# Optimization experiments

Hardware: AMD Instinct MI355X
Metric: run time of the kernel (lower is better)

## Reference

```python
import jax, jax.numpy as jnp
import numpy as np

N_NODES = 50000
N_EDGES = 800000
NUM_GRAPHS = 256
IN = 128
HID = 256
NUM_CLASSES = 10
EPS = 1e-5


def _glorot(key, shape):
    fan_in, fan_out = shape[0], shape[1]
    lim = (6.0 / (fan_in + fan_out)) ** 0.5
    return jax.random.uniform(key, shape, jnp.float32, -lim, lim)


def setup_inputs() -> dict:
    key = jax.random.key(0)
    ks = jax.random.split(key, 32)
    x = jax.random.normal(ks[0], (N_NODES, IN), jnp.float32)
    edge_index = jax.random.randint(ks[1], (2, N_EDGES), 0, N_NODES, jnp.int64)
    batch = jnp.sort(jax.random.randint(ks[2], (N_NODES,), 0, NUM_GRAPHS, jnp.int64))
    h = IN // 2  # 64
    p = {
        "x": x, "edge_index": edge_index, "batch": batch,
        # SAGEConv: out = lin_l(mean_aggr(x_j)) + lin_r(x_i); lin_l has bias, lin_r none
        "W1l": _glorot(ks[3], (IN, h)), "b1l": jnp.zeros((h,), jnp.float32), "W1r": _glorot(ks[4], (IN, h)),
        "W2l": _glorot(ks[5], (h, h)), "b2l": jnp.zeros((h,), jnp.float32), "W2r": _glorot(ks[6], (h, h)),
        "W3l": _glorot(ks[7], (h, h)), "b3l": jnp.zeros((h,), jnp.float32), "W3r": _glorot(ks[8], (h, h)),
        "lin1_w": _glorot(ks[9], (h, HID)), "lin1_b": jnp.zeros((HID,), jnp.float32),
        "g1": jnp.ones((HID,), jnp.float32), "be1": jnp.zeros((HID,), jnp.float32),
        "lin2_w": _glorot(ks[10], (HID, HID // 2)), "lin2_b": jnp.zeros((HID // 2,), jnp.float32),
        "g2": jnp.ones((HID // 2,), jnp.float32), "be2": jnp.zeros((HID // 2,), jnp.float32),
        "lin3_w": _glorot(ks[11], (HID // 2, HID // 4)), "lin3_b": jnp.zeros((HID // 4,), jnp.float32),
        "g3": jnp.ones((HID // 4,), jnp.float32), "be3": jnp.zeros((HID // 4,), jnp.float32),
        "lin4_w": _glorot(ks[12], (HID // 4, NUM_CLASSES)), "lin4_b": jnp.zeros((NUM_CLASSES,), jnp.float32),
    }
    return p


def sage_conv(x, src, dst, Wl, bl, Wr):
    # mean aggregation of source-node messages at destination nodes
    msg = x[src]  # [E, d] gather
    agg = jax.ops.segment_sum(msg, dst, num_segments=N_NODES)
    cnt = jax.ops.segment_sum(jnp.ones((src.shape[0],), x.dtype), dst, num_segments=N_NODES)
    agg = agg / jnp.maximum(cnt, 1.0)[:, None]
    return agg @ Wl + bl + x @ Wr


def batch_norm(x, gamma, beta):
    # training-mode BN (batch statistics, biased variance) as in torch default
    mean = jnp.mean(x, axis=0)
    var = jnp.mean((x - mean) ** 2, axis=0)
    return (x - mean) / jnp.sqrt(var + EPS) * gamma + beta


def reference(x, edge_index, batch,
              W1l, b1l, W1r, W2l, b2l, W2r, W3l, b3l, W3r,
              lin1_w, lin1_b, g1, be1, lin2_w, lin2_b, g2, be2,
              lin3_w, lin3_b, g3, be3, lin4_w, lin4_b):
    src, dst = edge_index[0], edge_index[1]
    h = sage_conv(x, src, dst, W1l, b1l, W1r)
    h = sage_conv(h, src, dst, W2l, b2l, W2r)
    h = sage_conv(h, src, dst, W3l, b3l, W3r)
    # global_mean_pool over graphs
    s = jax.ops.segment_sum(h, batch, num_segments=NUM_GRAPHS)
    n = jax.ops.segment_sum(jnp.ones((h.shape[0],), h.dtype), batch, num_segments=NUM_GRAPHS)
    c = s / jnp.maximum(n, 1.0)[:, None]
    # dropout is identity (self.training = False)
    c = jnp.tanh(batch_norm(c @ lin1_w + lin1_b, g1, be1))
    c = jnp.tanh(batch_norm(c @ lin2_w + lin2_b, g2, be2))
    c = jnp.tanh(batch_norm(c @ lin3_w + lin3_b, g3, be3))
    return c @ lin4_w + lin4_b
```

## Files before the change

kernel.cpp:

```cpp
#include <hip/hip_runtime.h>
#include <hip/hip_bf16.h>

#define N_NODES   50000
#define N_EDGES   800000
#define NUM_GRAPHS 256
#define IN_DIM    128
#define HD        64
#define EPS       1e-5f
#define SCAN_NB   196
#define NB_HEAD   64

typedef __hip_bfloat16 bf16;

__global__ void k_diag(float* __restrict__ out, int n, float v) {
    int t = blockIdx.x * 256 + threadIdx.x;
    if (t < n) out[t] = v;
}

__global__ void k_count(const int* __restrict__ dst, const int* __restrict__ batch,
                        int* __restrict__ cnti, int* __restrict__ pos,
                        int* __restrict__ gb) {
    int e = blockIdx.x * 256 + threadIdx.x;
    if (e < N_EDGES) pos[e] = atomicAdd(&cnti[dst[e]], 1);
    if (e < N_NODES) {
        int bg = batch[e];
        int bnext = (e + 1 < N_NODES) ? batch[e + 1] : NUM_GRAPHS;
        if (e == 0) {
            for (int g = 0; g <= bg; ++g) gb[g] = 0;
        }
        for (int g = bg + 1; g <= bnext; ++g) gb[g] = e + 1;
    }
}

__global__ void k_scan1(const int* __restrict__ cnti, int* __restrict__ off,
                        int* __restrict__ bsum) {
    __shared__ int wsum[4];
    int idx = blockIdx.x * 256 + threadIdx.x;
    int lane = threadIdx.x & 63, wid = threadIdx.x >> 6;
    int v = (idx < N_NODES) ? cnti[idx] : 0;
    int s = v;
    #pragma unroll
    for (int o = 1; o < 64; o <<= 1) {
        int u = __shfl_up(s, o);
        if (lane >= o) s += u;
    }
    if (lane == 63) wsum[wid] = s;
    __syncthreads();
    int wbase = 0;
    #pragma unroll
    for (int w = 0; w < 4; w++) wbase += (w < wid) ? wsum[w] : 0;
    if (idx < N_NODES) off[idx] = wbase + s - v;
    if (threadIdx.x == 255) bsum[blockIdx.x] = wbase + s;
}

__global__ void k_scan3(int* __restrict__ off, const int* __restrict__ bsum) {
    __shared__ int wsum[4];
    __shared__ int spre;
    int lane = threadIdx.x & 63, wid = threadIdx.x >> 6;
    int v = (threadIdx.x < blockIdx.x) ? bsum[threadIdx.x] : 0;
    #pragma unroll
    for (int o = 32; o > 0; o >>= 1) v += __shfl_down(v, o);
    if (lane == 0) wsum[wid] = v;
    __syncthreads();
    if (threadIdx.x == 0) spre = wsum[0] + wsum[1] + wsum[2] + wsum[3];
    __syncthreads();
    int pre = spre;
    int idx = blockIdx.x * 256 + threadIdx.x;
    if (idx < N_NODES) off[idx] += pre;
    else if (idx == N_NODES) off[N_NODES] = N_EDGES;
}

__global__ void k_fill(const int* __restrict__ src, const int* __restrict__ dst,
                       const int* __restrict__ off, const int* __restrict__ pos,
                       int* __restrict__ nbr) {
    int e = blockIdx.x * 256 + threadIdx.x;
    if (e >= N_EDGES) return;
    int d = dst[e];
    nbr[off[d] + pos[e]] = src[e];
}

template <int K>
__global__ __launch_bounds__(256) void k_xform3(
        const float* __restrict__ X, const float* __restrict__ Wl,
        const float* __restrict__ Wr, const float* __restrict__ bl,
        bf16* __restrict__ B, float* __restrict__ C) {
    __shared__ float tile[32 * K];
    const int NPW = 8;
    int nodes0 = blockIdx.x * 32;
    {
        const int total4 = 32 * K / 4;
        int nmax4 = (N_NODES - nodes0) * K / 4;
        const float4* Xg = (const float4*)(X + (long)nodes0 * K);
        float4* tg = (float4*)tile;
        for (int idx = threadIdx.x; idx < total4; idx += 256) {
            float4 v = make_float4(0.f, 0.f, 0.f, 0.f);
            if (idx < nmax4) v = Xg[idx];
            tg[idx] = v;
        }
    }
    __syncthreads();
    int wave = threadIdx.x >> 6, j = threadIdx.x & 63;
    long base = (long)nodes0 + wave * NPW;
    if (base >= N_NODES) return;
    float accB[NPW], accC[NPW];
    #pragma unroll
    for (int n = 0; n < NPW; n++) { accB[n] = 0.f; accC[n] = 0.f; }
    const float* Xs = tile + (wave * NPW) * K;
    for (int kc = 0; kc < K; kc += 4) {
        float wl0 = Wl[(kc + 0) * HD + j], wr0 = Wr[(kc + 0) * HD + j];
        float wl1 = Wl[(kc + 1) * HD + j], wr1 = Wr[(kc + 1) * HD + j];
        float wl2 = Wl[(kc + 2) * HD + j], wr2 = Wr[(kc + 2) * HD + j];
        float wl3 = Wl[(kc + 3) * HD + j], wr3 = Wr[(kc + 3) * HD + j];
        #pragma unroll
        for (int n = 0; n < NPW; n++) {
            float4 xv = *(const float4*)(Xs + n * K + kc);
            accB[n] = fmaf(xv.x, wl0, accB[n]);
            accC[n] = fmaf(xv.x, wr0, accC[n]);
            accB[n] = fmaf(xv.y, wl1, accB[n]);
            accC[n] = fmaf(xv.y, wr1, accC[n]);
            accB[n] = fmaf(xv.z, wl2, accB[n]);
            accC[n] = fmaf(xv.z, wr2, accC[n]);
            accB[n] = fmaf(xv.w, wl3, accB[n]);
            accC[n] = fmaf(xv.w, wr3, accC[n]);
        }
    }
    float bb = bl[j];
    int nact = (int)min((long)NPW, (long)N_NODES - base);
    for (int n = 0; n < nact; n++) {
        long i = base + n;
        B[i * HD + j] = __float2bfloat16(accB[n]);
        C[i * HD + j] = accC[n] + bb;
    }
}

__device__ __forceinline__ float bflo(unsigned u) { return __uint_as_float(u << 16); }
__device__ __forceinline__ float bfhi(unsigned u) { return __uint_as_float(u & 0xffff0000u); }

__global__ void k_gather(const int* __restrict__ off, const int* __restrict__ nbr,
                         const bf16* __restrict__ Bm, float* __restrict__ C) {
    int t = blockIdx.x * 256 + threadIdx.x;
    int i = t >> 6, lane = t & 63;
    if (i >= N_NODES) return;
    int half = lane >> 5, c = lane & 31;
    const unsigned* B2 = (const unsigned*)Bm;
    int beg = off[i], end = off[i + 1];
    float e0 = 0.f, e1 = 0.f, e2 = 0.f, e3 = 0.f;
    float e4 = 0.f, e5 = 0.f, e6 = 0.f, e7 = 0.f;
    float o0 = 0.f, o1 = 0.f, o2 = 0.f, o3 = 0.f;
    float o4 = 0.f, o5 = 0.f, o6 = 0.f, o7 = 0.f;
    for (int base = beg; base < end; base += 64) {
        int idx = base + lane;
        int nv = (idx < end) ? nbr[idx] : 0;
        int m = min(64, end - base);
        int tt = 0;
        for (; tt + 16 <= m; tt += 16) {
            int n0 = __shfl(nv, tt + 0 + half);
            int n1 = __shfl(nv, tt + 2 + half);
            int n2 = __shfl(nv, tt + 4 + half);
            int n3 = __shfl(nv, tt + 6 + half);
            int n4 = __shfl(nv, tt + 8 + half);
            int n5 = __shfl(nv, tt + 10 + half);
            int n6 = __shfl(nv, tt + 12 + half);
            int n7 = __shfl(nv, tt + 14 + half);
            unsigned u0 = B2[(long)n0 * 32 + c];
            unsigned u1 = B2[(long)n1 * 32 + c];
            unsigned u2 = B2[(long)n2 * 32 + c];
            unsigned u3 = B2[(long)n3 * 32 + c];
            unsigned u4 = B2[(long)n4 * 32 + c];
            unsigned u5 = B2[(long)n5 * 32 + c];
            unsigned u6 = B2[(long)n6 * 32 + c];
            unsigned u7 = B2[(long)n7 * 32 + c];
            e0 += bflo(u0); o0 += bfhi(u0);
            e1 += bflo(u1); o1 += bfhi(u1);
            e2 += bflo(u2); o2 += bfhi(u2);
            e3 += bflo(u3); o3 += bfhi(u3);
            e4 += bflo(u4); o4 += bfhi(u4);
            e5 += bflo(u5); o5 += bfhi(u5);
            e6 += bflo(u6); o6 += bfhi(u6);
            e7 += bflo(u7); o7 += bfhi(u7);
        }
        for (; tt + 2 <= m; tt += 2) {
            int n0 = __shfl(nv, tt + half);
            unsigned u0 = B2[(long)n0 * 32 + c];
            e0 += bflo(u0); o0 += bfhi(u0);
        }
        if (tt < m) {
            int n0 = __shfl(nv, tt);
            if (half == 0) {
                unsigned u0 = B2[(long)n0 * 32 + c];
                e0 += bflo(u0); o0 += bfhi(u0);
            }
        }
    }
    float es = ((e0 + e1) + (e2 + e3)) + ((e4 + e5) + (e6 + e7));
    float os = ((o0 + o1) + (o2 + o3)) + ((o4 + o5) + (o6 + o7));
    es += __shfl(es, lane ^ 32);
    os += __shfl(os, lane ^ 32);
    if (half == 0) {
        int deg = end - beg;
        float inv = 1.0f / (float)max(deg, 1);
        float2* Cp = (float2*)(C + (long)i * HD + 2 * c);
        float2 cur = *Cp;
        cur.x += es * inv;
        cur.y += os * inv;
        *Cp = cur;
    }
}

__device__ __forceinline__ void gbar(int* bar, int round) {
    __syncthreads();
    if (threadIdx.x == 0) {
        __threadfence();
        __hip_atomic_fetch_add(bar, 1, __ATOMIC_RELEASE, __HIP_MEMORY_SCOPE_AGENT);
        int target = round * NB_HEAD;
        while (__hip_atomic_load(bar, __ATOMIC_ACQUIRE, __HIP_MEMORY_SCOPE_AGENT) < target) {}
        __threadfence();
    }
    __syncthreads();
}

template <int N, int K, int C>
__device__ __forceinline__ void lin_stage(
        const float* __restrict__ A, const float* __restrict__ W,
        const float* __restrict__ bia, const float* __restrict__ gam,
        const float* __restrict__ bet, float* __restrict__ out,
        float* s_sum, float* s_sq, float* s_m, float* s_sc) {
    const int NRG = 256 / C;
    int t = threadIdx.x;
    int jj = t & (C - 1);
    int rg = t / C;
    int j = blockIdx.x * C + jj;
    float vals[C];
    float bj = bia[j];
    #pragma unroll
    for (int i = 0; i < C; i++) vals[i] = bj;
    #pragma unroll 8
    for (int k = 0; k < K; k += 4) {
        float w0 = W[(k + 0) * N + j];
        float w1 = W[(k + 1) * N + j];
        float w2 = W[(k + 2) * N + j];
        float w3 = W[(k + 3) * N + j];
        #pragma unroll
        for (int i = 0; i < C; i++) {
            int r = rg + NRG * i;
            float4 a = *(const float4*)(A + r * K + k);
            vals[i] = fmaf(a.x, w0, vals[i]);
            vals[i] = fmaf(a.y, w1, vals[i]);
            vals[i] = fmaf(a.z, w2, vals[i]);
            vals[i] = fmaf(a.w, w3, vals[i]);
        }
    }
    float sum = 0.f, sq = 0.f;
    #pragma unroll
    for (int i = 0; i < C; i++) { sum += vals[i]; sq += vals[i] * vals[i]; }
    int lane = t & 63, wid = t >> 6;
    #pragma unroll
    for (int o = C; o < 64; o <<= 1) {
        sum += __shfl_xor(sum, o);
        sq  += __shfl_xor(sq, o);
    }
    if (lane < C) { s_sum[wid * C + lane] = sum; s_sq[wid * C + lane] = sq; }
    __syncthreads();
    if (t < C) {
        float S = s_sum[t] + s_sum[C + t] + s_sum[2 * C + t] + s_sum[3 * C + t];
        float Q = s_sq[t]  + s_sq[C + t]  + s_sq[2 * C + t]  + s_sq[3 * C + t];
        float mean = S * (1.0f / NUM_GRAPHS);
        float var = Q * (1.0f / NUM_GRAPHS) - mean * mean;
        s_m[t] = mean;
        s_sc[t] = rsqrtf(fmaxf(var, 0.f) + EPS) * gam[blockIdx.x * C + t];
    }
    __syncthreads();
    float mean = s_m[jj], sc = s_sc[jj], sh = bet[j];
    #pragma unroll
    for (int i = 0; i < C; i++) {
        out[(rg + NRG * i) * N + j] = tanhf((vals[i] - mean) * sc + sh);
    }
}

__global__ __launch_bounds__(256) void k_head(
        const int* __restrict__ gb, const float* __restrict__ h, int* bar,
        const float* __restrict__ l1w, const float* __restrict__ l1b,
        const float* __restrict__ g1, const float* __restrict__ be1,
        const float* __restrict__ l2w, const float* __restrict__ l2b,
        const float* __restrict__ g2, const float* __restrict__ be2,
        const float* __restrict__ l3w, const float* __restrict__ l3b,
        const float* __restrict__ g3, const float* __restrict__ be3,
        const float* __restrict__ w4, const float* __restrict__ b4,
        float* __restrict__ cb, float* __restrict__ m1,
        float* __restrict__ m2, float* __restrict__ m3,
        float* __restrict__ out) {
    __shared__ float s_sum[16], s_sq[16], s_m[4], s_sc[4];
    int t = threadIdx.x, lane = t & 63, wid = t >> 6;

    {
        int g = blockIdx.x * 4 + wid;
        int beg = gb[g], end = gb[g + 1];
        float s0 = 0.f, s1 = 0.f, s2 = 0.f, s3 = 0.f;
        int n = beg;
        for (; n + 4 <= end; n += 4) {
            s0 += h[(long)(n + 0) * HD + lane];
            s1 += h[(long)(n + 1) * HD + lane];
            s2 += h[(long)(n + 2) * HD + lane];
            s3 += h[(long)(n + 3) * HD + lane];
        }
        for (; n < end; n++) s0 += h[(long)n * HD + lane];
        float tot = (s0 + s1) + (s2 + s3);
        cb[g * HD + lane] = tot / (float)max(end - beg, 1);
    }
    gbar(bar, 1);
    lin_stage<256, 64, 4>(cb, l1w, l1b, g1, be1, m1, s_sum, s_sq, s_m, s_sc);
    gbar(bar, 2);
    lin_stage<128, 256, 2>(m1, l2w, l2b, g2, be2, m2, s_sum, s_sq, s_m, s_sc);
    gbar(bar, 3);
    lin_stage<64, 128, 1>(m2, l3w, l3b, g3, be3, m3, s_sum, s_sq, s_m, s_sc);
    gbar(bar, 4);
    if (t < 40) {
        int q = t / 10, jf = t % 10;
        int row = blockIdx.x * 4 + q;
        const float* rp = m3 + row * 64;
        float s = b4[jf];
        #pragma unroll
        for (int k = 0; k < 64; k++) s = fmaf(rp[k], w4[k * 10 + jf], s);
        out[row * 10 + jf] = s;
    }
}

extern "C" void kernel_launch(void* const* d_in, const int* in_sizes, int n_in,
                              void* d_out, int out_size, void* d_ws, size_t ws_size,
                              hipStream_t stream) {
    const float* x     = (const float*)d_in[0];
    const int*   ei    = (const int*) d_in[1];
    const int*   batch = (const int*) d_in[2];
    const float *W1l = (const float*)d_in[3],  *b1l = (const float*)d_in[4],  *W1r = (const float*)d_in[5];
    const float *W2l = (const float*)d_in[6],  *b2l = (const float*)d_in[7],  *W2r = (const float*)d_in[8];
    const float *W3l = (const float*)d_in[9],  *b3l = (const float*)d_in[10], *W3r = (const float*)d_in[11];
    const float *lin1_w = (const float*)d_in[12], *lin1_b = (const float*)d_in[13];
    const float *g1 = (const float*)d_in[14], *be1 = (const float*)d_in[15];
    const float *lin2_w = (const float*)d_in[16], *lin2_b = (const float*)d_in[17];
    const float *g2 = (const float*)d_in[18], *be2 = (const float*)d_in[19];
    const float *lin3_w = (const float*)d_in[20], *lin3_b = (const float*)d_in[21];
    const float *g3 = (const float*)d_in[22], *be3 = (const float*)d_in[23];
    const float *lin4_w = (const float*)d_in[24], *lin4_b = (const float*)d_in[25];

    const int* srcp = ei;
    const int* dstp = ei + N_EDGES;

    const long NF = (long)N_NODES * HD;
    char* wsb  = (char*)d_ws;
    int*  cnti = (int*)wsb;
    int*  bar  = cnti + 50048;
    int*  pos  = bar  + 8;
    int*  off  = pos  + 800000;
    int*  nbr  = off  + 50056;
    int*  bsum = nbr  + 800000;
    int*  gb   = bsum + 256;
    bf16* B    = (bf16*)(gb + 264);
    float* H1  = (float*)(B + NF);
    float* H2  = H1  + NF;
    float* cb  = H2  + NF;
    float* m1  = cb  + NUM_GRAPHS * HD;
    float* m2  = m1  + NUM_GRAPHS * 256;
    float* m3  = m2  + NUM_GRAPHS * 128;
    float* endp= m3  + NUM_GRAPHS * 64;

    const size_t NEED = (size_t)((char*)endp - wsb);
    if (ws_size < NEED) {
        k_diag<<<(out_size + 255) / 256, 256, 0, stream>>>((float*)d_out, out_size,
                                                           (float)(ws_size >> 20));
        return;
    }

    const int TB = 256;
    const int gNE = (N_EDGES + TB - 1) / TB;
    const int gNF = (int)((NF + TB - 1) / TB);
    const int gXB = (N_NODES + 31) / 32;

    hipMemsetAsync(cnti, 0, (50048 + 8) * sizeof(int), stream);

    k_count<<<gNE, TB, 0, stream>>>(dstp, batch, cnti, pos, gb);
    k_scan1<<<SCAN_NB, TB, 0, stream>>>(cnti, off, bsum);
    k_scan3<<<SCAN_NB, TB, 0, stream>>>(off, bsum);
    k_fill<<<gNE, TB, 0, stream>>>(srcp, dstp, off, pos, nbr);

    k_xform3<IN_DIM><<<gXB, TB, 0, stream>>>(x, W1l, W1r, b1l, B, H1);
    k_gather<<<gNF, TB, 0, stream>>>(off, nbr, B, H1);
    k_xform3<HD><<<gXB, TB, 0, stream>>>(H1, W2l, W2r, b2l, B, H2);
    k_gather<<<gNF, TB, 0, stream>>>(off, nbr, B, H2);
    k_xform3<HD><<<gXB, TB, 0, stream>>>(H2, W3l, W3r, b3l, B, H1);
    k_gather<<<gNF, TB, 0, stream>>>(off, nbr, B, H1);

    k_head<<<NB_HEAD, TB, 0, stream>>>(gb, H1, bar,
                                       lin1_w, lin1_b, g1, be1,
                                       lin2_w, lin2_b, g2, be2,
                                       lin3_w, lin3_b, g3, be3,
                                       lin4_w, lin4_b,
                                       cb, m1, m2, m3, (float*)d_out);
}
```

Baseline: 414.4 us.

## Fuse global mean pooling into last gather via per-block atomic accumulation

The final gather kernel now adds its per-node results straight into the per-graph pooled buffer. Each block pre-reduces its four nodes and issues atomics, scaled by a per-graph inverse count computed in the scan kernel. This removes the pooling pass and one grid barrier from the head kernel, and avoids writing the last hidden layer and reading it back. The cost is an extra memset, float atomics with nondeterministic summation order, and an added block sync in the gather. The LAST path reads off[i+1] and batch[i] without a bounds guard, so the trailing threads of the final block may read past the end of these arrays.

```diff
diff --git a/kernel.cpp b/kernel.cpp
--- a/kernel.cpp
+++ b/kernel.cpp
@@ -53,7 +53,8 @@
     if (threadIdx.x == 255) bsum[blockIdx.x] = wbase + s;
 }
 
-__global__ void k_scan3(int* __restrict__ off, const int* __restrict__ bsum) {
+__global__ void k_scan3(int* __restrict__ off, const int* __restrict__ bsum,
+                        const int* __restrict__ gb, float* __restrict__ invc) {
     __shared__ int wsum[4];
     __shared__ int spre;
     int lane = threadIdx.x & 63, wid = threadIdx.x >> 6;
@@ -68,6 +69,10 @@
     int idx = blockIdx.x * 256 + threadIdx.x;
     if (idx < N_NODES) off[idx] += pre;
     else if (idx == N_NODES) off[N_NODES] = N_EDGES;
+    if (blockIdx.x == 0 && threadIdx.x < NUM_GRAPHS) {
+        int c0 = gb[threadIdx.x], c1 = gb[threadIdx.x + 1];
+        invc[threadIdx.x] = 1.0f / (float)max(c1 - c0, 1);
+    }
 }
 
 __global__ void k_fill(const int* __restrict__ src, const int* __restrict__ dst,
@@ -136,12 +141,16 @@
 __device__ __forceinline__ float bflo(unsigned u) { return __uint_as_float(u << 16); }
 __device__ __forceinline__ float bfhi(unsigned u) { return __uint_as_float(u & 0xffff0000u); }
 
+template <bool LAST>
 __global__ void k_gather(const int* __restrict__ off, const int* __restrict__ nbr,
-                         const bf16* __restrict__ Bm, float* __restrict__ C) {
+                         const bf16* __restrict__ Bm, float* __restrict__ C,
+                         const int* __restrict__ batch, const float* __restrict__ invc,
+                         float* __restrict__ cb) {
     int t = blockIdx.x * 256 + threadIdx.x;
     int i = t >> 6, lane = t & 63;
-    if (i >= N_NODES) return;
+    if (!LAST && i >= N_NODES) return;
     int half = lane >> 5, c = lane & 31;
+    int wid = threadIdx.x >> 6;
     const unsigned* B2 = (const unsigned*)Bm;
     int beg = off[i], end = off[i + 1];
     float e0 = 0.f, e1 = 0.f, e2 = 0.f, e3 = 0.f;
@@ -196,14 +205,42 @@
     float os = ((o0 + o1) + (o2 + o3)) + ((o4 + o5) + (o6 + o7));
     es += __shfl(es, lane ^ 32);
     os += __shfl(os, lane ^ 32);
-    if (half == 0) {
-        int deg = end - beg;
-        float inv = 1.0f / (float)max(deg, 1);
-        float2* Cp = (float2*)(C + (long)i * HD + 2 * c);
-        float2 cur = *Cp;
-        cur.x += es * inv;
-        cur.y += os * inv;
-        *Cp = cur;
+    if (!LAST) {
+        if (half == 0) {
+            int deg = end - beg;
+            float inv = 1.0f / (float)max(deg, 1);
+            float2* Cp = (float2*)(C + (long)i * HD + 2 * c);
+            float2 cur = *Cp;
+            cur.x += es * inv;
+            cur.y += os * inv;
+            *Cp = cur;
+        }
+    } else {
+        __shared__ float red[4][64];
+        __shared__ int gid[4];
+        if (half == 0) {
+            int deg = end - beg;
+            float inv = 1.0f / (float)max(deg, 1);
+            const float2 cur = *(const float2*)(C + (long)i * HD + 2 * c);
+            red[wid][2 * c]     = cur.x + es * inv;
+            red[wid][2 * c + 1] = cur.y + os * inv;
+        }
+        if (lane == 0) gid[wid] = batch[i];
+        __syncthreads();
+        if (wid == 0) {
+            int g0 = gid[0], g1 = gid[1], g2 = gid[2], g3 = gid[3];
+            float v0 = red[0][lane], v1 = red[1][lane];
+            float v2 = red[2][lane], v3 = red[3][lane];
+            if (g0 == g3) {
+                atomicAdd(&cb[g0 * HD + lane],
+                          ((v0 + v1) + (v2 + v3)) * invc[g0]);
+            } else {
+                atomicAdd(&cb[g0 * HD + lane], v0 * invc[g0]);
+                atomicAdd(&cb[g1 * HD + lane], v1 * invc[g1]);
+                atomicAdd(&cb[g2 * HD + lane], v2 * invc[g2]);
+                atomicAdd(&cb[g3 * HD + lane], v3 * invc[g3]);
+            }
+        }
     }
 }
 
@@ -275,10 +312,11 @@
     for (int i = 0; i < C; i++) {
         out[(rg + NRG * i) * N + j] = tanhf((vals[i] - mean) * sc + sh);
     }
+    __syncthreads();
 }
 
 __global__ __launch_bounds__(256) void k_head(
-        const int* __restrict__ gb, const float* __restrict__ h, int* bar,
+        int* bar,
         const float* __restrict__ l1w, const float* __restrict__ l1b,
         const float* __restrict__ g1, const float* __restrict__ be1,
         const float* __restrict__ l2w, const float* __restrict__ l2b,
@@ -286,34 +324,17 @@
         const float* __restrict__ l3w, const float* __restrict__ l3b,
         const float* __restrict__ g3, const float* __restrict__ be3,
         const float* __restrict__ w4, const float* __restrict__ b4,
-        float* __restrict__ cb, float* __restrict__ m1,
+        const float* __restrict__ cb, float* __restrict__ m1,
         float* __restrict__ m2, float* __restrict__ m3,
         float* __restrict__ out) {
     __shared__ float s_sum[16], s_sq[16], s_m[4], s_sc[4];
-    int t = threadIdx.x, lane = t & 63, wid = t >> 6;
-
-    {
-        int g = blockIdx.x * 4 + wid;
-        int beg = gb[g], end = gb[g + 1];
-        float s0 = 0.f, s1 = 0.f, s2 = 0.f, s3 = 0.f;
-        int n = beg;
-        for (; n + 4 <= end; n += 4) {
-            s0 += h[(long)(n + 0) * HD + lane];
-            s1 += h[(long)(n + 1) * HD + lane];
-            s2 += h[(long)(n + 2) * HD + lane];
-            s3 += h[(long)(n + 3) * HD + lane];
-        }
-        for (; n < end; n++) s0 += h[(long)n * HD + lane];
-        float tot = (s0 + s1) + (s2 + s3);
-        cb[g * HD + lane] = tot / (float)max(end - beg, 1);
-    }
+    int t = threadIdx.x;
+    lin_stage<256, 64, 4>(cb, l1w, l1b, g1, be1, m1, s_sum, s_sq, s_m, s_sc);
     gbar(bar, 1);
-    lin_stage<256, 64, 4>(cb, l1w, l1b, g1, be1, m1, s_sum, s_sq, s_m, s_sc);
+    lin_stage<128, 256, 2>(m1, l2w, l2b, g2, be2, m2, s_sum, s_sq, s_m, s_sc);
     gbar(bar, 2);
-    lin_stage<128, 256, 2>(m1, l2w, l2b, g2, be2, m2, s_sum, s_sq, s_m, s_sc);
+    lin_stage<64, 128, 1>(m2, l3w, l3b, g3, be3, m3, s_sum, s_sq, s_m, s_sc);
     gbar(bar, 3);
-    lin_stage<64, 128, 1>(m2, l3w, l3b, g3, be3, m3, s_sum, s_sq, s_m, s_sc);
-    gbar(bar, 4);
     if (t < 40) {
         int q = t / 10, jf = t % 10;
         int row = blockIdx.x * 4 + q;
@@ -354,7 +375,8 @@
     int*  nbr  = off  + 50056;
     int*  bsum = nbr  + 800000;
     int*  gb   = bsum + 256;
-    bf16* B    = (bf16*)(gb + 264);
+    float* invc = (float*)(gb + 264);
+    bf16* B    = (bf16*)(invc + 256);
     float* H1  = (float*)(B + NF);
     float* H2  = H1  + NF;
     float* cb  = H2  + NF;
@@ -376,20 +398,21 @@
     const int gXB = (N_NODES + 31) / 32;
 
     hipMemsetAsync(cnti, 0, (50048 + 8) * sizeof(int), stream);
+    hipMemsetAsync(cb, 0, NUM_GRAPHS * HD * sizeof(float), stream);
 
     k_count<<<gNE, TB, 0, stream>>>(dstp, batch, cnti, pos, gb);
     k_scan1<<<SCAN_NB, TB, 0, stream>>>(cnti, off, bsum);
-    k_scan3<<<SCAN_NB, TB, 0, stream>>>(off, bsum);
+    k_scan3<<<SCAN_NB, TB, 0, stream>>>(off, bsum, gb, invc);
     k_fill<<<gNE, TB, 0, stream>>>(srcp, dstp, off, pos, nbr);
 
     k_xform3<IN_DIM><<<gXB, TB, 0, stream>>>(x, W1l, W1r, b1l, B, H1);
-    k_gather<<<gNF, TB, 0, stream>>>(off, nbr, B, H1);
+    k_gather<false><<<gNF, TB, 0, stream>>>(off, nbr, B, H1, batch, invc, cb);
     k_xform3<HD><<<gXB, TB, 0, stream>>>(H1, W2l, W2r, b2l, B, H2);
-    k_gather<<<gNF, TB, 0, stream>>>(off, nbr, B, H2);
+    k_gather<false><<<gNF, TB, 0, stream>>>(off, nbr, B, H2, batch, invc, cb);
     k_xform3<HD><<<gXB, TB, 0, stream>>>(H2, W3l, W3r, b3l, B, H1);
-    k_gather<<<gNF, TB, 0, stream>>>(off, nbr, B, H1);
-
-    k_head<<<NB_HEAD, TB, 0, stream>>>(gb, H1, bar,
+    k_gather<true><<<gNF, TB, 0, stream>>>(off, nbr, B, H1, batch, invc, cb);
+
+    k_head<<<NB_HEAD, TB, 0, stream>>>(bar,
                                        lin1_w, lin1_b, g1, be1,
                                        lin2_w, lin2_b, g2, be2,
                                        lin3_w, lin3_b, g3, be3,
```

Result: faster. 401.1 us (-3.2%).
